# Kernel optimization log

Measured on AMD Instinct MI355X. Metric: run time of the kernel, lower is better.

Reference implementation:

```python
import jax, jax.numpy as jnp
import numpy as np

EMBED_DIM = 768
NUM_HEAD = 12
HEAD_DIM = EMBED_DIM // NUM_HEAD


def setup_inputs() -> dict:
    key = jax.random.key(0)
    ks = jax.random.split(key, 9)
    B, S, E = 1, 4096, EMBED_DIM
    s = 1.0 / np.sqrt(E)
    inp = {
        "x": jax.random.normal(ks[0], (B, S, E), dtype=jnp.float32),
        "mask": jnp.zeros((B, S), dtype=jnp.bool_),  # True = masked out (padding)
        "Wq": jax.random.normal(ks[1], (E, E), dtype=jnp.float32) * s,
        "bq": jnp.zeros((E,), dtype=jnp.float32),
        "Wk": jax.random.normal(ks[2], (E, E), dtype=jnp.float32) * s,
        "bk": jnp.zeros((E,), dtype=jnp.float32),
        "Wv": jax.random.normal(ks[3], (E, E), dtype=jnp.float32) * s,
        "bv": jnp.zeros((E,), dtype=jnp.float32),
        "Wo": jax.random.normal(ks[4], (E, E), dtype=jnp.float32) * s,
        "bo": jnp.zeros((E,), dtype=jnp.float32),
    }
    return inp


def reference(x, mask, Wq, bq, Wk, bk, Wv, bv, Wo, bo):
    B, S, E = x.shape
    H, D = NUM_HEAD, HEAD_DIM
    # QKV projections -> [B, H, S, D]
    q = (x @ Wq.T + bq).reshape(B, S, H, D).transpose(0, 2, 1, 3)
    k = (x @ Wk.T + bk).reshape(B, S, H, D).transpose(0, 2, 1, 3)
    v = (x @ Wv.T + bv).reshape(B, S, H, D).transpose(0, 2, 1, 3)
    # NOTE: original scales by sqrt(embed_dim), not sqrt(head_dim)
    attn = jnp.einsum("bhqd,bhkd->bhqk", q, k) / jnp.sqrt(jnp.float32(E))
    # mask: [B, S] -> broadcast over (head, query) dims; True -> -inf
    attn = jnp.where(mask[:, None, None, :], -jnp.inf, attn)
    attn = jax.nn.softmax(attn, axis=-1)  # same math as manual max-subtract softmax
    out = jnp.einsum("bhqk,bhkd->bhqd", attn, v)  # [B, H, S, D]
    out = out.transpose(0, 2, 1, 3).reshape(B, S, E)
    return out @ Wo.T + bo
```

## Files before the change

### kernel.cpp

```cpp
#include <hip/hip_runtime.h>
#include <hip/hip_bf16.h>
#include <math.h>

typedef __bf16 bf16;
typedef __attribute__((ext_vector_type(8))) __bf16 bf16x8;
typedef __attribute__((ext_vector_type(4))) __bf16 bf16x4;
typedef __attribute__((ext_vector_type(4))) float f32x4;

typedef __attribute__((address_space(1))) void* as1ptr;
typedef __attribute__((address_space(3))) void* as3ptr;

__device__ __forceinline__ void gload16(const void* g, void* lds) {
  __builtin_amdgcn_global_load_lds((as1ptr)(unsigned long long)(g),
                                   (as3ptr)(unsigned long long)(lds), 16, 0, 0);
}

#define MFMA16(a, b, c) __builtin_amdgcn_mfma_f32_16x16x32_bf16((a), (b), (c), 0, 0, 0)
#define EXP2(x) __builtin_amdgcn_exp2f(x)

#define SEQ 4096
#define EMB 768
#define QSC (0.036084391824351615f * 1.4426950408889634f)

#define NCVT 2688
__global__ __launch_bounds__(256)
void cvt_all_kernel(const float* __restrict__ x, const float* __restrict__ Wq,
                    const float* __restrict__ Wk, const float* __restrict__ Wv,
                    const float* __restrict__ Wo,
                    bf16* __restrict__ xb, bf16* __restrict__ Wqb, bf16* __restrict__ Wkb,
                    bf16* __restrict__ Wvb, bf16* __restrict__ Wob,
                    const unsigned char* __restrict__ mask, unsigned char* __restrict__ tf) {
  int b = blockIdx.x;
  if (b == NCVT) {
    int t = threadIdx.x;
    if (t < 64) {
      unsigned v = 0;
      const unsigned char* mp = mask + t * 64;
      for (int i = 0; i < 64; i++) v |= mp[i];
      tf[t] = (unsigned char)(v ? 1 : 0);
    }
    return;
  }
  const float* in;
  bf16* out;
  int base;
  if (b < 1536) {
    in = x; out = xb; base = b;
  } else {
    int r = b - 1536, seg = r / 288, off = r % 288;
    in  = (seg == 0) ? Wq  : (seg == 1) ? Wk  : (seg == 2) ? Wv  : Wo;
    out = (seg == 0) ? Wqb : (seg == 1) ? Wkb : (seg == 2) ? Wvb : Wob;
    base = off;
  }
  int i = (base * 256 + threadIdx.x) * 8;
  float4 a = *(const float4*)(in + i);
  float4 c = *(const float4*)(in + i + 4);
  bf16x8 v;
  v[0] = (bf16)a.x; v[1] = (bf16)a.y; v[2] = (bf16)a.z; v[3] = (bf16)a.w;
  v[4] = (bf16)c.x; v[5] = (bf16)c.y; v[6] = (bf16)c.z; v[7] = (bf16)c.w;
  *(bf16x8*)(out + i) = v;
}

template <int MODE>
__global__ __launch_bounds__(256)
void gemm_bt_kernel(const bf16* __restrict__ A,
                    const bf16* __restrict__ B0, const bf16* __restrict__ B1,
                    const bf16* __restrict__ B2,
                    const float* __restrict__ bias0, const float* __restrict__ bias1,
                    const float* __restrict__ bias2,
                    float* __restrict__ outF, bf16* __restrict__ Qh,
                    char* __restrict__ Kswz, char* __restrict__ Vswz) {
  __shared__ __attribute__((aligned(16))) char Asb[8192];
  __shared__ __attribute__((aligned(16))) char Bsb[8192];
  const int tid = threadIdx.x;
  const int wid = tid >> 6, lane = tid & 63;
  const int g = lane >> 4, c16 = lane & 15;
  const int wr = wid >> 1, wc = wid & 1;
  const int bm0 = blockIdx.x * 128;

  const bf16* Bp;
  const float* bias;
  int nb, mat = 0;
  if (MODE == 1) {
    mat = blockIdx.y / 6;
    nb = (blockIdx.y % 6) * 128;
    Bp = (mat == 0) ? B0 : (mat == 1 ? B1 : B2);
    bias = (mat == 0) ? bias0 : (mat == 1 ? bias1 : bias2);
  } else {
    nb = blockIdx.y * 128;
    Bp = B0;
    bias = bias0;
  }

  f32x4 acc[4][4];
#pragma unroll
  for (int i = 0; i < 4; i++)
#pragma unroll
    for (int j = 0; j < 4; j++) acc[i][j] = f32x4{0.f, 0.f, 0.f, 0.f};

  for (int kk = 0; kk < EMB / 32; ++kk) {
    __syncthreads();
#pragma unroll
    for (int c = 0; c < 2; ++c) {
      int ob = c * 4096 + tid * 16;
      int row = ob >> 6, colb = ob & 63;
      gload16((const char*)A + (size_t)(bm0 + row) * (EMB * 2) + kk * 64 + colb,
              Asb + c * 4096 + wid * 1024);
      gload16((const char*)Bp + (size_t)(nb + row) * (EMB * 2) + kk * 64 + colb,
              Bsb + c * 4096 + wid * 1024);
    }
    __syncthreads();
    bf16x8 a[4], b[4];
#pragma unroll
    for (int i = 0; i < 4; i++)
      a[i] = *(const bf16x8*)(Asb + (wr * 64 + i * 16 + c16) * 64 + g * 16);
#pragma unroll
    for (int j = 0; j < 4; j++)
      b[j] = *(const bf16x8*)(Bsb + (wc * 64 + j * 16 + c16) * 64 + g * 16);
#pragma unroll
    for (int i = 0; i < 4; i++)
#pragma unroll
      for (int j = 0; j < 4; j++) acc[i][j] = MFMA16(a[i], b[j], acc[i][j]);
  }

#pragma unroll
  for (int i = 0; i < 4; i++) {
#pragma unroll
    for (int j = 0; j < 4; j++) {
      int colL = nb + wc * 64 + j * 16 + c16;
      float bval = bias[colL];
#pragma unroll
      for (int r = 0; r < 4; r++) {
        int row = bm0 + wr * 64 + i * 16 + 4 * g + r;
        float val = acc[i][j][r] + bval;
        if (MODE == 0) {
          outF[(size_t)row * EMB + colL] = val;
        } else {
          int hh = colL >> 6, d = colL & 63;
          if (mat == 0) {
            Qh[((size_t)hh * SEQ + row) * 64 + d] = (bf16)(val * QSC);
          } else if (mat == 1) {
            *(bf16*)(Kswz + ((size_t)hh * SEQ + row) * 128 +
                     ((d * 2) ^ ((row & 7) << 4))) = (bf16)val;
          } else {
            int u5 = 8 * ((row & 15) >> 2) + 4 * ((row >> 4) & 1) + (row & 3);
            int cc = (row & 32) | u5;
            *(bf16*)(Vswz + ((size_t)hh * 64 + d) * 8192 + (size_t)(row >> 6) * 128 +
                     ((cc * 2) ^ ((d & 7) << 4))) = (bf16)val;
          }
        }
      }
    }
  }
}

__global__ __launch_bounds__(256)
void attn_kernel(const char* __restrict__ Kswz, const char* __restrict__ Vswz,
                 const bf16* __restrict__ Qh, const unsigned char* __restrict__ mask,
                 const unsigned char* __restrict__ tf, bf16* __restrict__ O) {
  __shared__ __attribute__((aligned(16))) char Kt[2][8192];
  __shared__ __attribute__((aligned(16))) char Vt[2][8192];
  const int tid = threadIdx.x;
  const int wid = tid >> 6, lane = tid & 63;
  const int g = (lane >> 4) & 3, c16 = lane & 15;
  const int h = blockIdx.y;
  const int q0 = blockIdx.x * 64 + wid * 16;

  bf16x8 qa0, qa1;
  {
    const bf16* qp = Qh + ((size_t)h * SEQ + q0 + c16) * 64 + g * 8;
    qa0 = *(const bf16x8*)(qp);
    qa1 = *(const bf16x8*)(qp + 32);
  }

  f32x4 ot[4];
#pragma unroll
  for (int f = 0; f < 4; ++f) ot[f] = f32x4{0.f, 0.f, 0.f, 0.f};
  float m_ = -1e38f, l_ = 0.f;

  const char* ksrc = Kswz + (size_t)h * SEQ * 128 + tid * 16;
  const char* vsrc0 = Vswz + ((size_t)h * 64 + (tid >> 3)) * 8192 + (tid & 7) * 16;
  const char* vsrc1 = Vswz + ((size_t)h * 64 + 32 + (tid >> 3)) * 8192 + (tid & 7) * 16;

#define STAGE(t, b)                                                    \
  do {                                                                 \
    gload16(ksrc + (size_t)(t)*8192,        &Kt[b][wid * 1024]);       \
    gload16(ksrc + (size_t)(t)*8192 + 4096, &Kt[b][4096 + wid * 1024]);\
    gload16(vsrc0 + (size_t)(t)*128, &Vt[b][wid * 1024]);              \
    gload16(vsrc1 + (size_t)(t)*128, &Vt[b][4096 + wid * 1024]);       \
  } while (0)

  STAGE(0, 0);
  __syncthreads();

  for (int t = 0; t < SEQ / 64; ++t) {
    const int b = t & 1;
    if (t < SEQ / 64 - 1) STAGE(t + 1, b ^ 1);
    const char* Kb = Kt[b];
    const char* Vb = Vt[b];

    f32x4 sc[4];
#pragma unroll
    for (int cf = 0; cf < 4; ++cf) {
      int row = cf * 16 + c16, sw = (row & 7) << 4;
      bf16x8 k0 = *(const bf16x8*)(Kb + row * 128 + ((g * 16) ^ sw));
      bf16x8 k1 = *(const bf16x8*)(Kb + row * 128 + ((64 + g * 16) ^ sw));
      f32x4 z = f32x4{0.f, 0.f, 0.f, 0.f};
      z = MFMA16(k0, qa0, z);
      z = MFMA16(k1, qa1, z);
      sc[cf] = z;
    }

    if (tf[t]) {
#pragma unroll
      for (int cf = 0; cf < 4; ++cf)
#pragma unroll
        for (int r = 0; r < 4; r++)
          if (mask[t * 64 + cf * 16 + 4 * g + r]) sc[cf][r] = -INFINITY;
    }

    float x0 = fmaxf(fmaxf(sc[0][0], sc[0][1]), fmaxf(sc[0][2], sc[0][3]));
    float x1 = fmaxf(fmaxf(sc[1][0], sc[1][1]), fmaxf(sc[1][2], sc[1][3]));
    float x2 = fmaxf(fmaxf(sc[2][0], sc[2][1]), fmaxf(sc[2][2], sc[2][3]));
    float x3 = fmaxf(fmaxf(sc[3][0], sc[3][1]), fmaxf(sc[3][2], sc[3][3]));
    float mt = fmaxf(fmaxf(x0, x1), fmaxf(x2, x3));
    mt = fmaxf(mt, __shfl_xor(mt, 16));
    mt = fmaxf(mt, __shfl_xor(mt, 32));

    if (__any(mt > m_ + 8.f)) {
      float mn = fmaxf(m_, mt);
      float corr = EXP2(m_ - mn);
      l_ *= corr;
#pragma unroll
      for (int f = 0; f < 4; ++f) ot[f] *= corr;
      m_ = mn;
    }

    float p[16];
#pragma unroll
    for (int cf = 0; cf < 4; ++cf)
#pragma unroll
      for (int r = 0; r < 4; r++) p[cf * 4 + r] = EXP2(sc[cf][r] - m_);
    l_ += ((p[0] + p[1]) + (p[2] + p[3])) + ((p[4] + p[5]) + (p[6] + p[7])) +
          (((p[8] + p[9]) + (p[10] + p[11])) + ((p[12] + p[13]) + (p[14] + p[15])));
    bf16x8 pb0, pb1;
#pragma unroll
    for (int e = 0; e < 8; ++e) {
      pb0[e] = (bf16)p[e];
      pb1[e] = (bf16)p[8 + e];
    }

#pragma unroll
    for (int f = 0; f < 4; ++f) {
      int row = f * 16 + c16, sw = (row & 7) << 4;
      bf16x8 v0 = *(const bf16x8*)(Vb + row * 128 + ((g * 16) ^ sw));
      bf16x8 v1 = *(const bf16x8*)(Vb + row * 128 + ((64 + g * 16) ^ sw));
      ot[f] = MFMA16(v0, pb0, ot[f]);
      ot[f] = MFMA16(v1, pb1, ot[f]);
    }
    __syncthreads();
  }
#undef STAGE

  l_ += __shfl_xor(l_, 16);
  l_ += __shfl_xor(l_, 32);
  float inv = 1.f / l_;
#pragma unroll
  for (int f = 0; f < 4; ++f) {
    bf16x4 w;
#pragma unroll
    for (int r = 0; r < 4; r++) w[r] = (bf16)(ot[f][r] * inv);
    *(bf16x4*)(O + (size_t)(q0 + c16) * EMB + h * 64 + f * 16 + 4 * g) = w;
  }
}

extern "C" void kernel_launch(void* const* d_in, const int* in_sizes, int n_in,
                              void* d_out, int out_size, void* d_ws, size_t ws_size,
                              hipStream_t stream) {
  (void)in_sizes; (void)n_in; (void)out_size; (void)ws_size;
  const float* x = (const float*)d_in[0];
  const unsigned char* mask = (const unsigned char*)d_in[1];
  const float* Wq = (const float*)d_in[2];
  const float* bq = (const float*)d_in[3];
  const float* Wk = (const float*)d_in[4];
  const float* bk = (const float*)d_in[5];
  const float* Wv = (const float*)d_in[6];
  const float* bv = (const float*)d_in[7];
  const float* Wo = (const float*)d_in[8];
  const float* bo = (const float*)d_in[9];
  float* out = (float*)d_out;
  char* ws = (char*)d_ws;

  bf16* xb   = (bf16*)(ws + 0);
  bf16* Wqb  = (bf16*)(ws + 6291456);
  bf16* Wkb  = (bf16*)(ws + 7471104);
  bf16* Wvb  = (bf16*)(ws + 8650752);
  bf16* Wob  = (bf16*)(ws + 9830400);
  bf16* Qh   = (bf16*)(ws + 11010048);
  char* Kswz = ws + 17301504;
  char* Vswz = ws + 23592960;
  bf16* Obuf = (bf16*)(ws + 29884416);
  unsigned char* tf = (unsigned char*)(ws + 36175872);

  cvt_all_kernel<<<NCVT + 1, 256, 0, stream>>>(x, Wq, Wk, Wv, Wo, xb, Wqb, Wkb, Wvb,
                                               Wob, mask, tf);
  gemm_bt_kernel<1><<<dim3(32, 18), 256, 0, stream>>>(
      xb, Wqb, Wkb, Wvb, bq, bk, bv, nullptr, Qh, Kswz, Vswz);
  attn_kernel<<<dim3(64, 12), 256, 0, stream>>>(Kswz, Vswz, Qh, mask, tf, Obuf);
  gemm_bt_kernel<0><<<dim3(32, 6), 256, 0, stream>>>(
      Obuf, Wob, nullptr, nullptr, bo, nullptr, nullptr, out, nullptr, nullptr, nullptr);
}
```

Measured before the change: 147.9 us.

## Triple-buffer LDS staging with vmcnt waits and MFMA priority in GEMM and attention

Both the GEMM and attention kernels move from single or double buffering to a three-stage ring of LDS buffers. Each iteration waits only on the older async loads (vmcnt(4)) and uses one barrier instead of two __syncthreads. MFMA blocks are wrapped in s_setprio raises, and the per-tile mask flags are packed into one 64-bit ballot word. The aim is to hide global-load latency behind compute and cut barrier stalls, at the cost of more LDS per block, which may lower occupancy.

Measured after the change: 144.2 us. 2.5% less time.

```diff
diff --git a/kernel.cpp b/kernel.cpp
--- a/kernel.cpp
+++ b/kernel.cpp
@@ -17,6 +17,11 @@
 
 #define MFMA16(a, b, c) __builtin_amdgcn_mfma_f32_16x16x32_bf16((a), (b), (c), 0, 0, 0)
 #define EXP2(x) __builtin_amdgcn_exp2f(x)
+#define WAITV4 asm volatile("s_waitcnt vmcnt(4)" ::: "memory")
+#define WAITV0 asm volatile("s_waitcnt vmcnt(0)" ::: "memory")
+#define BAR() __builtin_amdgcn_s_barrier()
+#define PRIO1() __builtin_amdgcn_s_setprio(1)
+#define PRIO0() __builtin_amdgcn_s_setprio(0)
 
 #define SEQ 4096
 #define EMB 768
@@ -29,7 +34,8 @@
                     const float* __restrict__ Wo,
                     bf16* __restrict__ xb, bf16* __restrict__ Wqb, bf16* __restrict__ Wkb,
                     bf16* __restrict__ Wvb, bf16* __restrict__ Wob,
-                    const unsigned char* __restrict__ mask, unsigned char* __restrict__ tf) {
+                    const unsigned char* __restrict__ mask,
+                    unsigned long long* __restrict__ tf64) {
   int b = blockIdx.x;
   if (b == NCVT) {
     int t = threadIdx.x;
@@ -37,7 +43,8 @@
       unsigned v = 0;
       const unsigned char* mp = mask + t * 64;
       for (int i = 0; i < 64; i++) v |= mp[i];
-      tf[t] = (unsigned char)(v ? 1 : 0);
+      unsigned long long bits = __ballot(v != 0);
+      if (t == 0) *tf64 = bits;
     }
     return;
   }
@@ -70,8 +77,8 @@
                     const float* __restrict__ bias2,
                     float* __restrict__ outF, bf16* __restrict__ Qh,
                     char* __restrict__ Kswz, char* __restrict__ Vswz) {
-  __shared__ __attribute__((aligned(16))) char Asb[8192];
-  __shared__ __attribute__((aligned(16))) char Bsb[8192];
+  __shared__ __attribute__((aligned(16))) char Asb[3][8192];
+  __shared__ __attribute__((aligned(16))) char Bsb[3][8192];
   const int tid = threadIdx.x;
   const int wid = tid >> 6, lane = tid & 63;
   const int g = lane >> 4, c16 = lane & 15;
@@ -92,36 +99,58 @@
     bias = bias0;
   }
 
+  const int arow = tid >> 2, acol = (tid & 3) * 16;
+
+#define STAGE_G(k, b)                                                              \
+  do {                                                                             \
+    gload16((const char*)A + (size_t)(bm0 + arow) * (EMB * 2) + (k)*64 + acol,     \
+            &Asb[b][wid * 1024]);                                                  \
+    gload16((const char*)A + (size_t)(bm0 + 64 + arow) * (EMB * 2) + (k)*64 + acol,\
+            &Asb[b][4096 + wid * 1024]);                                           \
+    gload16((const char*)Bp + (size_t)(nb + arow) * (EMB * 2) + (k)*64 + acol,     \
+            &Bsb[b][wid * 1024]);                                                  \
+    gload16((const char*)Bp + (size_t)(nb + 64 + arow) * (EMB * 2) + (k)*64 + acol,\
+            &Bsb[b][4096 + wid * 1024]);                                           \
+  } while (0)
+
   f32x4 acc[4][4];
 #pragma unroll
   for (int i = 0; i < 4; i++)
 #pragma unroll
     for (int j = 0; j < 4; j++) acc[i][j] = f32x4{0.f, 0.f, 0.f, 0.f};
 
-  for (int kk = 0; kk < EMB / 32; ++kk) {
-    __syncthreads();
-#pragma unroll
-    for (int c = 0; c < 2; ++c) {
-      int ob = c * 4096 + tid * 16;
-      int row = ob >> 6, colb = ob & 63;
-      gload16((const char*)A + (size_t)(bm0 + row) * (EMB * 2) + kk * 64 + colb,
-              Asb + c * 4096 + wid * 1024);
-      gload16((const char*)Bp + (size_t)(nb + row) * (EMB * 2) + kk * 64 + colb,
-              Bsb + c * 4096 + wid * 1024);
+#define COMPUTE_G(cur)                                                         \
+  do {                                                                         \
+    bf16x8 a[4], b[4];                                                         \
+    _Pragma("unroll") for (int i = 0; i < 4; i++)                              \
+        a[i] = *(const bf16x8*)(&Asb[cur][(wr * 64 + i * 16 + c16) * 64 + g * 16]); \
+    _Pragma("unroll") for (int j = 0; j < 4; j++)                              \
+        b[j] = *(const bf16x8*)(&Bsb[cur][(wc * 64 + j * 16 + c16) * 64 + g * 16]); \
+    PRIO1();                                                                   \
+    _Pragma("unroll") for (int i = 0; i < 4; i++)                              \
+        _Pragma("unroll") for (int j = 0; j < 4; j++)                          \
+            acc[i][j] = MFMA16(a[i], b[j], acc[i][j]);                         \
+    PRIO0();                                                                   \
+  } while (0)
+
+  STAGE_G(0, 0);
+  STAGE_G(1, 1);
+  int cur = 0;
+  for (int kk = 0; kk < EMB / 32 - 1; ++kk) {
+    WAITV4;
+    BAR();
+    if (kk < EMB / 32 - 2) {
+      int stb = (cur == 0) ? 2 : cur - 1;
+      STAGE_G(kk + 2, stb);
     }
-    __syncthreads();
-    bf16x8 a[4], b[4];
-#pragma unroll
-    for (int i = 0; i < 4; i++)
-      a[i] = *(const bf16x8*)(Asb + (wr * 64 + i * 16 + c16) * 64 + g * 16);
-#pragma unroll
-    for (int j = 0; j < 4; j++)
-      b[j] = *(const bf16x8*)(Bsb + (wc * 64 + j * 16 + c16) * 64 + g * 16);
-#pragma unroll
-    for (int i = 0; i < 4; i++)
-#pragma unroll
-      for (int j = 0; j < 4; j++) acc[i][j] = MFMA16(a[i], b[j], acc[i][j]);
-  }
+    COMPUTE_G(cur);
+    cur = (cur == 2) ? 0 : cur + 1;
+  }
+  WAITV0;
+  BAR();
+  COMPUTE_G(cur);
+#undef STAGE_G
+#undef COMPUTE_G
 
 #pragma unroll
   for (int i = 0; i < 4; i++) {
@@ -157,14 +186,15 @@
 __global__ __launch_bounds__(256)
 void attn_kernel(const char* __restrict__ Kswz, const char* __restrict__ Vswz,
                  const bf16* __restrict__ Qh, const unsigned char* __restrict__ mask,
-                 const unsigned char* __restrict__ tf, bf16* __restrict__ O) {
-  __shared__ __attribute__((aligned(16))) char Kt[2][8192];
-  __shared__ __attribute__((aligned(16))) char Vt[2][8192];
+                 const unsigned long long* __restrict__ tf64, bf16* __restrict__ O) {
+  __shared__ __attribute__((aligned(16))) char Kt[3][8192];
+  __shared__ __attribute__((aligned(16))) char Vt[3][8192];
   const int tid = threadIdx.x;
   const int wid = tid >> 6, lane = tid & 63;
   const int g = (lane >> 4) & 3, c16 = lane & 15;
   const int h = blockIdx.y;
   const int q0 = blockIdx.x * 64 + wid * 16;
+  const unsigned long long tfb = *tf64;
 
   bf16x8 qa0, qa1;
   {
@@ -190,77 +220,87 @@
     gload16(vsrc1 + (size_t)(t)*128, &Vt[b][4096 + wid * 1024]);       \
   } while (0)
 
+#define COMPUTE(t, cur)                                                         \
+  do {                                                                          \
+    const char* Kb = Kt[cur];                                                   \
+    const char* Vb = Vt[cur];                                                   \
+    f32x4 sc[4];                                                                \
+    bf16x8 k0[4], k1[4];                                                        \
+    _Pragma("unroll") for (int cf = 0; cf < 4; ++cf) {                          \
+      int row = cf * 16 + c16, sw = (row & 7) << 4;                             \
+      k0[cf] = *(const bf16x8*)(Kb + row * 128 + ((g * 16) ^ sw));              \
+      k1[cf] = *(const bf16x8*)(Kb + row * 128 + ((64 + g * 16) ^ sw));         \
+    }                                                                           \
+    PRIO1();                                                                    \
+    _Pragma("unroll") for (int cf = 0; cf < 4; ++cf) {                          \
+      f32x4 z = f32x4{0.f, 0.f, 0.f, 0.f};                                      \
+      z = MFMA16(k0[cf], qa0, z);                                               \
+      z = MFMA16(k1[cf], qa1, z);                                               \
+      sc[cf] = z;                                                               \
+    }                                                                           \
+    PRIO0();                                                                    \
+    if (tfb & (1ull << (t))) {                                                  \
+      _Pragma("unroll") for (int cf = 0; cf < 4; ++cf)                          \
+          _Pragma("unroll") for (int r = 0; r < 4; r++)                         \
+              if (mask[(t)*64 + cf * 16 + 4 * g + r]) sc[cf][r] = -INFINITY;    \
+    }                                                                           \
+    float x0 = fmaxf(fmaxf(sc[0][0], sc[0][1]), fmaxf(sc[0][2], sc[0][3]));     \
+    float x1 = fmaxf(fmaxf(sc[1][0], sc[1][1]), fmaxf(sc[1][2], sc[1][3]));     \
+    float x2 = fmaxf(fmaxf(sc[2][0], sc[2][1]), fmaxf(sc[2][2], sc[2][3]));     \
+    float x3 = fmaxf(fmaxf(sc[3][0], sc[3][1]), fmaxf(sc[3][2], sc[3][3]));     \
+    float mt = fmaxf(fmaxf(x0, x1), fmaxf(x2, x3));                             \
+    mt = fmaxf(mt, __shfl_xor(mt, 16));                                         \
+    mt = fmaxf(mt, __shfl_xor(mt, 32));                                         \
+    if (__any(mt > m_ + 8.f)) {                                                 \
+      float mn = fmaxf(m_, mt);                                                 \
+      float corr = EXP2(m_ - mn);                                               \
+      l_ *= corr;                                                               \
+      _Pragma("unroll") for (int f = 0; f < 4; ++f) ot[f] *= corr;              \
+      m_ = mn;                                                                  \
+    }                                                                           \
+    float p[16];                                                                \
+    _Pragma("unroll") for (int cf = 0; cf < 4; ++cf)                            \
+        _Pragma("unroll") for (int r = 0; r < 4; r++)                           \
+            p[cf * 4 + r] = EXP2(sc[cf][r] - m_);                               \
+    l_ += ((p[0] + p[1]) + (p[2] + p[3])) + ((p[4] + p[5]) + (p[6] + p[7])) +   \
+          (((p[8] + p[9]) + (p[10] + p[11])) + ((p[12] + p[13]) + (p[14] + p[15]))); \
+    bf16x8 pb0, pb1;                                                            \
+    _Pragma("unroll") for (int e = 0; e < 8; ++e) {                             \
+      pb0[e] = (bf16)p[e];                                                      \
+      pb1[e] = (bf16)p[8 + e];                                                  \
+    }                                                                           \
+    bf16x8 v0[4], v1[4];                                                        \
+    _Pragma("unroll") for (int f = 0; f < 4; ++f) {                             \
+      int row = f * 16 + c16, sw = (row & 7) << 4;                              \
+      v0[f] = *(const bf16x8*)(Vb + row * 128 + ((g * 16) ^ sw));               \
+      v1[f] = *(const bf16x8*)(Vb + row * 128 + ((64 + g * 16) ^ sw));          \
+    }                                                                           \
+    PRIO1();                                                                    \
+    _Pragma("unroll") for (int f = 0; f < 4; ++f) {                             \
+      ot[f] = MFMA16(v0[f], pb0, ot[f]);                                        \
+      ot[f] = MFMA16(v1[f], pb1, ot[f]);                                        \
+    }                                                                           \
+    PRIO0();                                                                    \
+  } while (0)
+
   STAGE(0, 0);
-  __syncthreads();
-
-  for (int t = 0; t < SEQ / 64; ++t) {
-    const int b = t & 1;
-    if (t < SEQ / 64 - 1) STAGE(t + 1, b ^ 1);
-    const char* Kb = Kt[b];
-    const char* Vb = Vt[b];
-
-    f32x4 sc[4];
-#pragma unroll
-    for (int cf = 0; cf < 4; ++cf) {
-      int row = cf * 16 + c16, sw = (row & 7) << 4;
-      bf16x8 k0 = *(const bf16x8*)(Kb + row * 128 + ((g * 16) ^ sw));
-      bf16x8 k1 = *(const bf16x8*)(Kb + row * 128 + ((64 + g * 16) ^ sw));
-      f32x4 z = f32x4{0.f, 0.f, 0.f, 0.f};
-      z = MFMA16(k0, qa0, z);
-      z = MFMA16(k1, qa1, z);
-      sc[cf] = z;
+  STAGE(1, 1);
+  int cur = 0;
+  for (int t = 0; t < SEQ / 64 - 1; ++t) {
+    WAITV4;
+    BAR();
+    if (t < SEQ / 64 - 2) {
+      int stb = (cur == 0) ? 2 : cur - 1;
+      STAGE(t + 2, stb);
     }
-
-    if (tf[t]) {
-#pragma unroll
-      for (int cf = 0; cf < 4; ++cf)
-#pragma unroll
-        for (int r = 0; r < 4; r++)
-          if (mask[t * 64 + cf * 16 + 4 * g + r]) sc[cf][r] = -INFINITY;
-    }
-
-    float x0 = fmaxf(fmaxf(sc[0][0], sc[0][1]), fmaxf(sc[0][2], sc[0][3]));
-    float x1 = fmaxf(fmaxf(sc[1][0], sc[1][1]), fmaxf(sc[1][2], sc[1][3]));
-    float x2 = fmaxf(fmaxf(sc[2][0], sc[2][1]), fmaxf(sc[2][2], sc[2][3]));
-    float x3 = fmaxf(fmaxf(sc[3][0], sc[3][1]), fmaxf(sc[3][2], sc[3][3]));
-    float mt = fmaxf(fmaxf(x0, x1), fmaxf(x2, x3));
-    mt = fmaxf(mt, __shfl_xor(mt, 16));
-    mt = fmaxf(mt, __shfl_xor(mt, 32));
-
-    if (__any(mt > m_ + 8.f)) {
-      float mn = fmaxf(m_, mt);
-      float corr = EXP2(m_ - mn);
-      l_ *= corr;
-#pragma unroll
-      for (int f = 0; f < 4; ++f) ot[f] *= corr;
-      m_ = mn;
-    }
-
-    float p[16];
-#pragma unroll
-    for (int cf = 0; cf < 4; ++cf)
-#pragma unroll
-      for (int r = 0; r < 4; r++) p[cf * 4 + r] = EXP2(sc[cf][r] - m_);
-    l_ += ((p[0] + p[1]) + (p[2] + p[3])) + ((p[4] + p[5]) + (p[6] + p[7])) +
-          (((p[8] + p[9]) + (p[10] + p[11])) + ((p[12] + p[13]) + (p[14] + p[15])));
-    bf16x8 pb0, pb1;
-#pragma unroll
-    for (int e = 0; e < 8; ++e) {
-      pb0[e] = (bf16)p[e];
-      pb1[e] = (bf16)p[8 + e];
-    }
-
-#pragma unroll
-    for (int f = 0; f < 4; ++f) {
-      int row = f * 16 + c16, sw = (row & 7) << 4;
-      bf16x8 v0 = *(const bf16x8*)(Vb + row * 128 + ((g * 16) ^ sw));
-      bf16x8 v1 = *(const bf16x8*)(Vb + row * 128 + ((64 + g * 16) ^ sw));
-      ot[f] = MFMA16(v0, pb0, ot[f]);
-      ot[f] = MFMA16(v1, pb1, ot[f]);
-    }
-    __syncthreads();
-  }
+    COMPUTE(t, cur);
+    cur = (cur == 2) ? 0 : cur + 1;
+  }
+  WAITV0;
+  BAR();
+  COMPUTE(SEQ / 64 - 1, cur);
 #undef STAGE
+#undef COMPUTE
 
   l_ += __shfl_xor(l_, 16);
   l_ += __shfl_xor(l_, 32);
@@ -300,13 +340,13 @@
   char* Kswz = ws + 17301504;
   char* Vswz = ws + 23592960;
   bf16* Obuf = (bf16*)(ws + 29884416);
-  unsigned char* tf = (unsigned char*)(ws + 36175872);
+  unsigned long long* tf64 = (unsigned long long*)(ws + 36175872);
 
   cvt_all_kernel<<<NCVT + 1, 256, 0, stream>>>(x, Wq, Wk, Wv, Wo, xb, Wqb, Wkb, Wvb,
-                                               Wob, mask, tf);
+                                               Wob, mask, tf64);
   gemm_bt_kernel<1><<<dim3(32, 18), 256, 0, stream>>>(
       xb, Wqb, Wkb, Wvb, bq, bk, bv, nullptr, Qh, Kswz, Vswz);
-  attn_kernel<<<dim3(64, 12), 256, 0, stream>>>(Kswz, Vswz, Qh, mask, tf, Obuf);
+  attn_kernel<<<dim3(64, 12), 256, 0, stream>>>(Kswz, Vswz, Qh, mask, tf64, Obuf);
   gemm_bt_kernel<0><<<dim3(32, 6), 256, 0, stream>>>(
       Obuf, Wob, nullptr, nullptr, bo, nullptr, nullptr, out, nullptr, nullptr, nullptr);
 }
```
